# Kernel optimization log

Measured on AMD Instinct MI355X. Metric: run time of the kernel, lower is better.

Reference implementation:

```python
import jax, jax.numpy as jnp
import jax.scipy as jsp
import numpy as np

NUM_EMBEDDINGS = 256
EMBEDDING_DIM = 64
SPARSITY_LEVEL = 4
N_BINS = 16
COEF_MAX = 3.0
COEF_MU = 50.0
COMMITMENT_COST = 0.25
EPSILON = 1e-10


def _normalize_dict(dictionary):
    # F.normalize(dict, p=2, dim=0, eps): x / max(||x||_2, eps) per column
    nrm = jnp.linalg.norm(dictionary, axis=0, keepdims=True)
    return dictionary / jnp.maximum(nrm, EPSILON)


def _quantize_coeff_mu_law(coeff):
    inv_log1p_mu = 1.0 / np.log1p(COEF_MU)  # scalar constant
    c = jnp.clip(coeff, -COEF_MAX, COEF_MAX) / COEF_MAX
    encoded = jnp.sign(c) * jnp.log1p(jnp.abs(c) * COEF_MU) * inv_log1p_mu
    scaled = (encoded + 1.0) * ((N_BINS - 1) / 2.0)
    bin_idx = jnp.clip(jnp.round(scaled).astype(jnp.int32), 0, N_BINS - 1)
    # dequantize
    z = bin_idx.astype(coeff.dtype) * (2.0 / (N_BINS - 1)) - 1.0
    decoded = jnp.sign(z) * (jnp.expm1(jnp.abs(z) / inv_log1p_mu) / COEF_MU) * COEF_MAX
    return bin_idx, decoded


def batch_omp_with_support(X, Dn, K):
    # X: [M, Bs] signals, Dn: [M, N] normalized dictionary
    G = Dn.T @ Dn                       # [N, N] Gram
    h_bar = (Dn.T @ X).T                # [Bs, N] correlations
    Bs, N = h_bar.shape
    dt = h_bar.dtype
    h = h_bar
    mask = jnp.zeros((Bs, N), dtype=bool)
    L = jnp.ones((Bs, 1, 1), dtype=dt)  # incremental Cholesky of G[I, I]
    I = jnp.zeros((Bs, 0), dtype=jnp.int32)
    x_sel = jnp.zeros((Bs, 0), dtype=dt)
    rows = jnp.arange(Bs)
    for k in range(1, K + 1):  # K is small & static -> unrolled
        idx = jnp.argmax(jnp.abs(h) * (~mask), axis=1).astype(jnp.int32)
        mask = mask.at[rows, idx].set(True)
        if k > 1:
            G_stack = G[I, idx[:, None]]                     # [Bs, k-1]
            w = jsp.linalg.solve_triangular(L, G_stack[..., None], lower=True)  # [Bs,k-1,1]
            wT = jnp.swapaxes(w, 1, 2)                       # [Bs,1,k-1]
            w_corner = jnp.sqrt(jnp.clip(1.0 - jnp.sum(wT * wT, axis=2, keepdims=True), 1e-12))
            top = jnp.concatenate([L, jnp.zeros((Bs, k - 1, 1), dt)], axis=2)
            bot = jnp.concatenate([wT, w_corner], axis=2)
            L = jnp.concatenate([top, bot], axis=1)          # [Bs,k,k]
        I = jnp.concatenate([I, idx[:, None]], axis=1)       # [Bs,k]
        h_stack = jnp.take_along_axis(h_bar, I, axis=1)[..., None]  # [Bs,k,1]
        # cholesky_solve: L L^T x = h
        y = jsp.linalg.solve_triangular(L, h_stack, lower=True)
        xs = jsp.linalg.solve_triangular(jnp.swapaxes(L, 1, 2), y, lower=False)
        x_sel = xs[..., 0]                                   # [Bs,k] coeffs aligned w/ support
        beta = jnp.einsum('bk,bkn->bn', x_sel, G[I])         # [Bs,N]
        h = h_bar - beta
    return I, x_sel


def setup_inputs() -> dict:
    key = jax.random.key(0)
    k1, k2 = jax.random.split(key)
    z_e = jax.random.normal(k1, (32, EMBEDDING_DIM, 64, 64), dtype=jnp.float32)
    dictionary = jax.random.normal(k2, (EMBEDDING_DIM, NUM_EMBEDDINGS), dtype=jnp.float32) * 0.02
    return {"z_e": z_e, "dictionary": dictionary}


def reference(z_e, dictionary):
    B, C, H, W = z_e.shape
    Dn = _normalize_dict(dictionary)
    signals = jnp.transpose(z_e, (0, 2, 3, 1)).reshape(-1, C).T  # [C, B*H*W]
    # OMP runs with no grad (torch.no_grad in original)
    support, coeffs = jax.lax.stop_gradient(
        batch_omp_with_support(jax.lax.stop_gradient(signals), jax.lax.stop_gradient(Dn), SPARSITY_LEVEL)
    )
    # mu-law quantize coefficients (constants w.r.t. grads)
    bin_idx, coeffs_q = _quantize_coeff_mu_law(coeffs)
    # reconstruct with quantized coeffs; dictionary path is differentiable
    atoms = Dn.T[support]                                    # [Bs, K, C]
    recon_flat = jnp.einsum('bkc,bk->bc', atoms, coeffs_q)
    recon = jnp.transpose(recon_flat.reshape(B, H, W, C), (0, 3, 1, 2))
    # VQ-VAE style losses + STE
    e_latent_loss = jnp.mean((jax.lax.stop_gradient(recon) - z_e) ** 2)
    q_latent_loss = jnp.mean((recon - jax.lax.stop_gradient(z_e)) ** 2)
    loss = q_latent_loss + COMMITMENT_COST * e_latent_loss
    z_q = z_e + jax.lax.stop_gradient(recon - z_e)
    return z_q, loss


if __name__ == '__main__':
    out = reference(**setup_inputs())
    print(out[0].shape, out[1])
```

## Files before the change

kernel.cpp:

```cpp
#include <hip/hip_runtime.h>
#include <math.h>

#define NEMB 256
#define DIM 64
#define SIGS 128
#define THREADS 512
#define NSIG 131072
#define GRID (NSIG / SIGS)

#define LOG1P50 3.9318256327243257
#define INV_MU_F ((float)(1.0 / LOG1P50))
#define TWO15_F ((float)(2.0 / 15.0))

#define LB_SIG   0
#define LB_XS    32768
#define LB_QI    34816
#define LB_RED   36864
#define LDS_BYTES 36928

__global__ void k_normalize(const float* __restrict__ D, float* __restrict__ Dn)
{
#pragma clang fp contract(off)
    int n = threadIdx.x;
    float ss = 0.0f;
    for (int c = 0; c < DIM; c++) {
        float v = D[c * NEMB + n];
        float sq = v * v;
        ss = ss + sq;
    }
    float nrm = fmaxf(sqrtf(ss), 1e-10f);
    for (int c = 0; c < DIM; c++)
        Dn[c * NEMB + n] = D[c * NEMB + n] / nrm;
}

__global__ void k_gram(const float* __restrict__ Dn, float* __restrict__ G)
{
    __shared__ float coli[DIM];
    int i = blockIdx.x, j = threadIdx.x;
    if (j < DIM) coli[j] = Dn[j * NEMB + i];
    __syncthreads();
    float s = 0.0f;
#pragma unroll
    for (int c = 0; c < DIM; c++) s = fmaf(coli[c], Dn[c * NEMB + j], s);
    G[i * NEMB + j] = s;
}

__device__ __forceinline__ float quant_decode(float coeff)
{
#pragma clang fp contract(off)
    float c = fminf(fmaxf(coeff, -3.0f), 3.0f) / 3.0f;
    float ac = fabsf(c);
    float sgn = (c > 0.0f) ? 1.0f : ((c < 0.0f) ? -1.0f : 0.0f);
    float l = log1pf(ac * 50.0f);
    float enc = (sgn * l) * INV_MU_F;
    float scaled = (enc + 1.0f) * 7.5f;
    int bin = (int)rintf(scaled);
    bin = bin < 0 ? 0 : (bin > 15 ? 15 : bin);
    float t = (float)bin * TWO15_F;
    float zv = t - 1.0f;
    float az = fabsf(zv);
    float sz = (zv > 0.0f) ? 1.0f : ((zv < 0.0f) ? -1.0f : 0.0f);
    float e = expm1f(az / INV_MU_F);
    return (sz * (e / 50.0f)) * 3.0f;
}

__device__ __forceinline__ void omp_signal(const float* hb4, int lane,
                                           const float* __restrict__ G,
                                           float* __restrict__ xsv,
                                           int* __restrict__ qi, int s)
{
#pragma clang fp contract(off)
    float hbsi[4] = {hb4[0], hb4[1], hb4[2], hb4[3]};
    float h[4] = {hbsi[0], hbsi[1], hbsi[2], hbsi[3]};
    float Lm[4][4];
    float Gr[3][4];
    int Iv[4];
    float hsel[4];
    float xs[4];
    float y[4];
    int m4 = 0;
#pragma unroll
    for (int kk = 0; kk < 4; kk++) {
        float bv = -1.0f;
        int bj = 0;
#pragma unroll
        for (int j = 0; j < 4; j++) {
            float v = (m4 & (1 << j)) ? 0.0f : fabsf(h[j]);
            if (v > bv) { bv = v; bj = j; }
        }
        float vmax = bv;
#pragma unroll
        for (int off = 1; off < 64; off <<= 1)
            vmax = fmaxf(vmax, __shfl_xor(vmax, off));
        unsigned long long mball = __ballot(bv == vmax);
        int owner = __ffsll(mball) - 1;
        int idx = __shfl(4 * lane + bj, owner);
        idx = __builtin_amdgcn_readfirstlane(idx);
        if (lane == owner) m4 |= (1 << bj);
        if (kk < 3) {
            const float4 gt = *(const float4*)(G + (size_t)idx * NEMB + 4 * lane);
            Gr[kk][0] = gt.x; Gr[kk][1] = gt.y; Gr[kk][2] = gt.z; Gr[kk][3] = gt.w;
        }
        if (kk > 0) {
            float Gs[3], w[3];
#pragma unroll
            for (int j = 0; j < 3; j++)
                if (j < kk) Gs[j] = G[(size_t)Iv[j] * NEMB + idx];
#pragma unroll
            for (int r = 0; r < 3; r++) {
                if (r < kk) {
                    float acc = 0.0f;
#pragma unroll
                    for (int cc = 0; cc < 3; cc++)
                        if (cc < r) { float p = Lm[r][cc] * w[cc]; acc = acc + p; }
                    float t2 = Gs[r] - acc;
                    w[r] = t2 / Lm[r][r];
                }
            }
            float ssum = 0.0f;
#pragma unroll
            for (int j = 0; j < 3; j++)
                if (j < kk) { float p = w[j] * w[j]; ssum = ssum + p; }
            float om = 1.0f - ssum;
            float wc = sqrtf(fmaxf(om, 1e-12f));
#pragma unroll
            for (int cc = 0; cc < 3; cc++)
                if (cc < kk) Lm[kk][cc] = w[cc];
            Lm[kk][kk] = wc;
        } else {
            Lm[0][0] = 1.0f;
        }
        Iv[kk] = idx;
        {
            float tv = (bj == 0) ? hbsi[0] : ((bj == 1) ? hbsi[1] : ((bj == 2) ? hbsi[2] : hbsi[3]));
            hsel[kk] = __shfl(tv, owner);
        }
        {
            float acc = 0.0f;
#pragma unroll
            for (int cc = 0; cc < 3; cc++)
                if (cc < kk) { float p = Lm[kk][cc] * y[cc]; acc = acc + p; }
            float t2 = hsel[kk] - acc;
            y[kk] = t2 / Lm[kk][kk];
        }
#pragma unroll
        for (int r = 3; r >= 0; r--) {
            if (r <= kk) {
                float acc = 0.0f;
#pragma unroll
                for (int cc = 0; cc < 4; cc++)
                    if (cc > r && cc <= kk) { float p = Lm[cc][r] * xs[cc]; acc = acc + p; }
                float t2 = y[r] - acc;
                xs[r] = t2 / Lm[r][r];
            }
        }
        if (kk < 3) {
#pragma unroll
            for (int j = 0; j < 4; j++) {
                float bsum = 0.0f;
#pragma unroll
                for (int jj = 0; jj < 3; jj++)
                    if (jj <= kk) { float p = xs[jj] * Gr[jj][j]; bsum = bsum + p; }
                h[j] = hbsi[j] - bsum;
            }
        }
    }
    if (lane == 0) {
#pragma unroll
        for (int j = 0; j < 4; j++) {
            xsv[j * SIGS + s] = xs[j];
            qi[j * SIGS + s] = Iv[j];
        }
    }
}

__launch_bounds__(THREADS, 6)
__global__ void k_omp(const float* __restrict__ z,
                      const float* __restrict__ Dn_g,
                      const float* __restrict__ G,
                      double* __restrict__ loss_acc,
                      float* __restrict__ zq)
{
    extern __shared__ char smem[];
    float* sig = (float*)(smem + LB_SIG);
    float* xsv = (float*)(smem + LB_XS);
    int* qi = (int*)(smem + LB_QI);
    double* red = (double*)(smem + LB_RED);

    int tid = threadIdx.x;
    int lane = tid & 63;
    int wid = tid >> 6;

    long sbase = (long)blockIdx.x * SIGS;
    int b = (int)(sbase >> 12);
    int pl0 = (int)(sbase & 4095);
    const float* zb = z + ((size_t)b << 18) + pl0;
    {
        int w = tid & (SIGS - 1);
        int g = tid >> 7;
#pragma unroll
        for (int i = 0; i < 16; i++) {
            int c = g * 16 + i;
            sig[c * SIGS + w] = zb[(size_t)c * 4096 + w];
        }
    }
    __syncthreads();

    for (int g2 = 0; g2 < 2; g2++) {
        int s0 = wid * 16 + g2 * 8;
        float hb[8][4];
#pragma unroll
        for (int a = 0; a < 8; a++)
#pragma unroll
            for (int t = 0; t < 4; t++) hb[a][t] = 0.0f;
#pragma unroll 8
        for (int c = 0; c < DIM; c++) {
            float4 sva = *(const float4*)(sig + c * SIGS + s0);
            float4 svb = *(const float4*)(sig + c * SIGS + s0 + 4);
            float s8[8] = {sva.x, sva.y, sva.z, sva.w, svb.x, svb.y, svb.z, svb.w};
            float4 dv = *(const float4*)(Dn_g + c * NEMB + 4 * lane);
            float d4[4] = {dv.x, dv.y, dv.z, dv.w};
#pragma unroll
            for (int a = 0; a < 8; a++) {
                hb[a][0] = fmaf(s8[a], d4[0], hb[a][0]);
                hb[a][1] = fmaf(s8[a], d4[1], hb[a][1]);
                hb[a][2] = fmaf(s8[a], d4[2], hb[a][2]);
                hb[a][3] = fmaf(s8[a], d4[3], hb[a][3]);
            }
        }
#pragma unroll
        for (int a = 0; a < 8; a++)
            omp_signal(hb[a], lane, G, xsv, qi, s0 + a);
    }
    __syncthreads();

    {
        int jq = tid >> 7;
        int wq = tid & (SIGS - 1);
        xsv[jq * SIGS + wq] = quant_decode(xsv[jq * SIGS + wq]);
    }
    __syncthreads();

    double lsum = 0.0;
    float* zqb = zq + ((size_t)b << 18) + pl0;
    {
#pragma clang fp contract(off)
        int w = tid & (SIGS - 1);
        int g = tid >> 7;
        float q0 = xsv[0 * SIGS + w], q1 = xsv[1 * SIGS + w];
        float q2 = xsv[2 * SIGS + w], q3 = xsv[3 * SIGS + w];
        int i0 = qi[0 * SIGS + w], i1 = qi[1 * SIGS + w];
        int i2 = qi[2 * SIGS + w], i3 = qi[3 * SIGS + w];
#pragma unroll
        for (int ci = 0; ci < 16; ci++) {
            int c = g * 16 + ci;
            const float* dr = Dn_g + c * NEMB;
            float p0 = q0 * dr[i0];
            float p1 = q1 * dr[i1];
            float p2 = q2 * dr[i2];
            float p3 = q3 * dr[i3];
            float r = p0 + p1;
            r = r + p2;
            r = r + p3;
            float zev = sig[c * SIGS + w];
            float d = r - zev;
            float zqv = zev + d;
            lsum += (double)d * (double)d;
            zqb[(size_t)c * 4096 + w] = zqv;
        }
    }
#pragma unroll
    for (int off = 32; off > 0; off >>= 1) lsum += __shfl_xor(lsum, off);
    if (lane == 0) red[wid] = lsum;
    __syncthreads();
    if (tid == 0) {
        double t = 0.0;
#pragma unroll
        for (int i = 0; i < 8; i++) t += red[i];
        atomicAdd(loss_acc, t);
    }
}

__global__ void k_final(const double* __restrict__ loss_acc, float* __restrict__ out)
{
    double m = loss_acc[0] / 8388608.0;
    out[0] = (float)(m + 0.25 * m);
}

extern "C" void kernel_launch(void* const* d_in, const int* in_sizes, int n_in,
                              void* d_out, int out_size, void* d_ws, size_t ws_size,
                              hipStream_t stream)
{
    const float* z = (const float*)d_in[0];
    const float* D = (const float*)d_in[1];
    float* out = (float*)d_out;
    char* ws = (char*)d_ws;
    double* loss_acc = (double*)ws;
    float* Dn = (float*)(ws + 256);
    float* G = (float*)(ws + 256 + 65536);

    hipMemsetAsync(loss_acc, 0, sizeof(double), stream);
    k_normalize<<<1, NEMB, 0, stream>>>(D, Dn);
    k_gram<<<NEMB, NEMB, 0, stream>>>(Dn, G);
    hipFuncSetAttribute(reinterpret_cast<const void*>(k_omp),
                        hipFuncAttributeMaxDynamicSharedMemorySize, LDS_BYTES);
    k_omp<<<GRID, THREADS, LDS_BYTES, stream>>>(z, Dn, G, loss_acc, out);
    k_final<<<1, 1, 0, stream>>>(loss_acc, out + 8388608);
    (void)in_sizes; (void)n_in; (void)out_size; (void)ws_size;
}
```

Measured before the change: 302.6 us.

## Interleave two OMP signals per wave with DPP reductions and packed FMA

Result: faster. 292.3 us (-3.4%).

```diff
diff --git a/kernel.cpp b/kernel.cpp
--- a/kernel.cpp
+++ b/kernel.cpp
@@ -18,10 +18,37 @@
 #define LB_RED   36864
 #define LDS_BYTES 36928
 
-__global__ void k_normalize(const float* __restrict__ D, float* __restrict__ Dn)
+typedef float f2 __attribute__((ext_vector_type(2)));
+
+__device__ __forceinline__ float rdlane_f(float v, int lane)
+{
+    return __builtin_bit_cast(float, __builtin_amdgcn_readlane(__builtin_bit_cast(int, v), lane));
+}
+
+template<int CTRL>
+__device__ __forceinline__ float dpp_fmax(float m)
+{
+    int sh = __builtin_amdgcn_update_dpp(0, __builtin_bit_cast(int, m), CTRL, 0xf, 0xf, true);
+    return fmaxf(m, __builtin_bit_cast(float, sh));
+}
+
+__device__ __forceinline__ float wave_max_nn(float v)
+{
+    v = dpp_fmax<0x111>(v);
+    v = dpp_fmax<0x112>(v);
+    v = dpp_fmax<0x114>(v);
+    v = dpp_fmax<0x118>(v);
+    v = dpp_fmax<0x142>(v);
+    v = dpp_fmax<0x143>(v);
+    return v;
+}
+
+__global__ void k_normalize(const float* __restrict__ D, float* __restrict__ Dn,
+                            double* __restrict__ loss_acc, unsigned int* __restrict__ ctr)
 {
 #pragma clang fp contract(off)
     int n = threadIdx.x;
+    if (n == 0) { loss_acc[0] = 0.0; ctr[0] = 0u; }
     float ss = 0.0f;
     for (int c = 0; c < DIM; c++) {
         float v = D[c * NEMB + n];
@@ -64,48 +91,84 @@
     return (sz * (e / 50.0f)) * 3.0f;
 }
 
-__device__ __forceinline__ void omp_signal(const float* hb4, int lane,
-                                           const float* __restrict__ G,
-                                           float* __restrict__ xsv,
-                                           int* __restrict__ qi, int s)
+__device__ __forceinline__ void omp_pair(const f2* hbA_in, const f2* hbB_in,
+                                         int lane, int hi,
+                                         const float* __restrict__ G,
+                                         float* __restrict__ xsv,
+                                         int* __restrict__ qi, int sA)
 {
 #pragma clang fp contract(off)
-    float hbsi[4] = {hb4[0], hb4[1], hb4[2], hb4[3]};
-    float h[4] = {hbsi[0], hbsi[1], hbsi[2], hbsi[3]};
+    f2 hbsiA[2] = {hbA_in[0], hbA_in[1]};
+    f2 hbsiB[2] = {hbB_in[0], hbB_in[1]};
+    f2 hA[2] = {hbsiA[0], hbsiA[1]};
+    f2 hB[2] = {hbsiB[0], hbsiB[1]};
+    f2 GrA[3][2], GrB[3][2];
     float Lm[4][4];
-    float Gr[3][4];
-    int Iv[4];
-    float hsel[4];
-    float xs[4];
-    float y[4];
-    int m4 = 0;
+    int IvA[4], IvB[4];
+    float y[4], xs[4];
+    int m4A = 0, m4B = 0;
 #pragma unroll
     for (int kk = 0; kk < 4; kk++) {
-        float bv = -1.0f;
-        int bj = 0;
+        float bvA = -1.0f, bvB = -1.0f;
+        int bjA = 0, bjB = 0;
 #pragma unroll
         for (int j = 0; j < 4; j++) {
-            float v = (m4 & (1 << j)) ? 0.0f : fabsf(h[j]);
-            if (v > bv) { bv = v; bj = j; }
-        }
-        float vmax = bv;
-#pragma unroll
-        for (int off = 1; off < 64; off <<= 1)
-            vmax = fmaxf(vmax, __shfl_xor(vmax, off));
-        unsigned long long mball = __ballot(bv == vmax);
-        int owner = __ffsll(mball) - 1;
-        int idx = __shfl(4 * lane + bj, owner);
-        idx = __builtin_amdgcn_readfirstlane(idx);
-        if (lane == owner) m4 |= (1 << bj);
+            float vA_ = (m4A & (1 << j)) ? 0.0f : fabsf(hA[j >> 1][j & 1]);
+            if (vA_ > bvA) { bvA = vA_; bjA = j; }
+            float vB_ = (m4B & (1 << j)) ? 0.0f : fabsf(hB[j >> 1][j & 1]);
+            if (vB_ > bvB) { bvB = vB_; bjB = j; }
+        }
+        float mA = wave_max_nn(bvA);
+        float mB = wave_max_nn(bvB);
+        float vmaxA = rdlane_f(mA, 63);
+        float vmaxB = rdlane_f(mB, 63);
+        unsigned long long ballA = __ballot(bvA == vmaxA);
+        unsigned long long ballB = __ballot(bvB == vmaxB);
+        int ownerA = __ffsll((long long)ballA) - 1;
+        int ownerB = __ffsll((long long)ballB) - 1;
+        int bjAo = __builtin_amdgcn_readlane(bjA, ownerA);
+        int bjBo = __builtin_amdgcn_readlane(bjB, ownerB);
+        int idxA = 4 * ownerA + bjAo;
+        int idxB = 4 * ownerB + bjBo;
+        m4A |= (lane == ownerA) ? (1 << bjAo) : 0;
+        m4B |= (lane == ownerB) ? (1 << bjBo) : 0;
+        IvA[kk] = idxA; IvB[kk] = idxB;
+        float tvA = hbsiA[0][0];
+        tvA = (bjA == 1) ? hbsiA[0][1] : tvA;
+        tvA = (bjA == 2) ? hbsiA[1][0] : tvA;
+        tvA = (bjA == 3) ? hbsiA[1][1] : tvA;
+        float tvB = hbsiB[0][0];
+        tvB = (bjB == 1) ? hbsiB[0][1] : tvB;
+        tvB = (bjB == 2) ? hbsiB[1][0] : tvB;
+        tvB = (bjB == 3) ? hbsiB[1][1] : tvB;
+        float hselA = rdlane_f(tvA, ownerA);
+        float hselB = rdlane_f(tvB, ownerB);
+        float hsel = hi ? hselB : hselA;
         if (kk < 3) {
-            const float4 gt = *(const float4*)(G + (size_t)idx * NEMB + 4 * lane);
-            Gr[kk][0] = gt.x; Gr[kk][1] = gt.y; Gr[kk][2] = gt.z; Gr[kk][3] = gt.w;
+            const float4 ga = *(const float4*)(G + ((size_t)idxA << 8) + 4 * lane);
+            const float4 gb = *(const float4*)(G + ((size_t)idxB << 8) + 4 * lane);
+            GrA[kk][0].x = ga.x; GrA[kk][0].y = ga.y;
+            GrA[kk][1].x = ga.z; GrA[kk][1].y = ga.w;
+            GrB[kk][0].x = gb.x; GrB[kk][0].y = gb.y;
+            GrB[kk][1].x = gb.z; GrB[kk][1].y = gb.w;
         }
         if (kk > 0) {
             float Gs[3], w[3];
 #pragma unroll
             for (int j = 0; j < 3; j++)
-                if (j < kk) Gs[j] = G[(size_t)Iv[j] * NEMB + idx];
+                if (j < kk) {
+                    float eA = GrA[j][0][0];
+                    eA = (bjAo == 1) ? GrA[j][0][1] : eA;
+                    eA = (bjAo == 2) ? GrA[j][1][0] : eA;
+                    eA = (bjAo == 3) ? GrA[j][1][1] : eA;
+                    float eB = GrB[j][0][0];
+                    eB = (bjBo == 1) ? GrB[j][0][1] : eB;
+                    eB = (bjBo == 2) ? GrB[j][1][0] : eB;
+                    eB = (bjBo == 3) ? GrB[j][1][1] : eB;
+                    float gA = rdlane_f(eA, ownerA);
+                    float gB = rdlane_f(eB, ownerB);
+                    Gs[j] = hi ? gB : gA;
+                }
 #pragma unroll
             for (int r = 0; r < 3; r++) {
                 if (r < kk) {
@@ -114,7 +177,7 @@
                     for (int cc = 0; cc < 3; cc++)
                         if (cc < r) { float p = Lm[r][cc] * w[cc]; acc = acc + p; }
                     float t2 = Gs[r] - acc;
-                    w[r] = t2 / Lm[r][r];
+                    w[r] = (r == 0) ? t2 : t2 / Lm[r][r];
                 }
             }
             float ssum = 0.0f;
@@ -130,18 +193,13 @@
         } else {
             Lm[0][0] = 1.0f;
         }
-        Iv[kk] = idx;
-        {
-            float tv = (bj == 0) ? hbsi[0] : ((bj == 1) ? hbsi[1] : ((bj == 2) ? hbsi[2] : hbsi[3]));
-            hsel[kk] = __shfl(tv, owner);
-        }
         {
             float acc = 0.0f;
 #pragma unroll
             for (int cc = 0; cc < 3; cc++)
                 if (cc < kk) { float p = Lm[kk][cc] * y[cc]; acc = acc + p; }
-            float t2 = hsel[kk] - acc;
-            y[kk] = t2 / Lm[kk][kk];
+            float t2 = hsel - acc;
+            y[kk] = (kk == 0) ? t2 : t2 / Lm[kk][kk];
         }
 #pragma unroll
         for (int r = 3; r >= 0; r--) {
@@ -151,35 +209,54 @@
                 for (int cc = 0; cc < 4; cc++)
                     if (cc > r && cc <= kk) { float p = Lm[cc][r] * xs[cc]; acc = acc + p; }
                 float t2 = y[r] - acc;
-                xs[r] = t2 / Lm[r][r];
+                xs[r] = (r == 0) ? t2 : t2 / Lm[r][r];
             }
         }
         if (kk < 3) {
-#pragma unroll
-            for (int j = 0; j < 4; j++) {
-                float bsum = 0.0f;
+            float xsA[4], xsB[4];
+#pragma unroll
+            for (int j = 0; j < 4; j++)
+                if (j <= kk) {
+                    xsA[j] = rdlane_f(xs[j], 0);
+                    xsB[j] = rdlane_f(xs[j], 32);
+                }
+#pragma unroll
+            for (int jp = 0; jp < 2; jp++) {
+                f2 bsA = {0.0f, 0.0f};
+                f2 bsB = {0.0f, 0.0f};
 #pragma unroll
                 for (int jj = 0; jj < 3; jj++)
-                    if (jj <= kk) { float p = xs[jj] * Gr[jj][j]; bsum = bsum + p; }
-                h[j] = hbsi[j] - bsum;
+                    if (jj <= kk) {
+                        f2 xa = {xsA[jj], xsA[jj]};
+                        f2 xb = {xsB[jj], xsB[jj]};
+                        f2 pA = xa * GrA[jj][jp];
+                        bsA = bsA + pA;
+                        f2 pB = xb * GrB[jj][jp];
+                        bsB = bsB + pB;
+                    }
+                hA[jp] = hbsiA[jp] - bsA;
+                hB[jp] = hbsiB[jp] - bsB;
             }
         }
     }
-    if (lane == 0) {
+    if ((lane & 31) == 0) {
+        int s = sA + hi;
 #pragma unroll
         for (int j = 0; j < 4; j++) {
             xsv[j * SIGS + s] = xs[j];
-            qi[j * SIGS + s] = Iv[j];
-        }
-    }
-}
-
-__launch_bounds__(THREADS, 6)
+            qi[j * SIGS + s] = hi ? IvB[j] : IvA[j];
+        }
+    }
+}
+
+__launch_bounds__(THREADS, 4)
 __global__ void k_omp(const float* __restrict__ z,
                       const float* __restrict__ Dn_g,
                       const float* __restrict__ G,
                       double* __restrict__ loss_acc,
-                      float* __restrict__ zq)
+                      unsigned int* __restrict__ ctr,
+                      float* __restrict__ zq,
+                      float* __restrict__ loss_out)
 {
     extern __shared__ char smem[];
     float* sig = (float*)(smem + LB_SIG);
@@ -189,6 +266,7 @@
 
     int tid = threadIdx.x;
     int lane = tid & 63;
+    int hi = lane >> 5;
     int wid = tid >> 6;
 
     long sbase = (long)blockIdx.x * SIGS;
@@ -208,29 +286,30 @@
 
     for (int g2 = 0; g2 < 2; g2++) {
         int s0 = wid * 16 + g2 * 8;
-        float hb[8][4];
-#pragma unroll
-        for (int a = 0; a < 8; a++)
-#pragma unroll
-            for (int t = 0; t < 4; t++) hb[a][t] = 0.0f;
+        f2 hb[8][2];
+#pragma unroll
+        for (int a = 0; a < 8; a++) {
+            hb[a][0] = (f2){0.0f, 0.0f};
+            hb[a][1] = (f2){0.0f, 0.0f};
+        }
 #pragma unroll 8
         for (int c = 0; c < DIM; c++) {
             float4 sva = *(const float4*)(sig + c * SIGS + s0);
             float4 svb = *(const float4*)(sig + c * SIGS + s0 + 4);
             float s8[8] = {sva.x, sva.y, sva.z, sva.w, svb.x, svb.y, svb.z, svb.w};
             float4 dv = *(const float4*)(Dn_g + c * NEMB + 4 * lane);
-            float d4[4] = {dv.x, dv.y, dv.z, dv.w};
+            f2 d0; d0.x = dv.x; d0.y = dv.y;
+            f2 d1; d1.x = dv.z; d1.y = dv.w;
 #pragma unroll
             for (int a = 0; a < 8; a++) {
-                hb[a][0] = fmaf(s8[a], d4[0], hb[a][0]);
-                hb[a][1] = fmaf(s8[a], d4[1], hb[a][1]);
-                hb[a][2] = fmaf(s8[a], d4[2], hb[a][2]);
-                hb[a][3] = fmaf(s8[a], d4[3], hb[a][3]);
+                f2 sa = {s8[a], s8[a]};
+                hb[a][0] = __builtin_elementwise_fma(sa, d0, hb[a][0]);
+                hb[a][1] = __builtin_elementwise_fma(sa, d1, hb[a][1]);
             }
         }
 #pragma unroll
-        for (int a = 0; a < 8; a++)
-            omp_signal(hb[a], lane, G, xsv, qi, s0 + a);
+        for (int p = 0; p < 4; p++)
+            omp_pair(hb[2 * p], hb[2 * p + 1], lane, hi, G, xsv, qi, s0 + 2 * p);
     }
     __syncthreads();
 
@@ -278,13 +357,13 @@
 #pragma unroll
         for (int i = 0; i < 8; i++) t += red[i];
         atomicAdd(loss_acc, t);
-    }
-}
-
-__global__ void k_final(const double* __restrict__ loss_acc, float* __restrict__ out)
-{
-    double m = loss_acc[0] / 8388608.0;
-    out[0] = (float)(m + 0.25 * m);
+        __threadfence();
+        unsigned int done = atomicAdd(ctr, 1u);
+        if (done == GRID - 1) {
+            double m = atomicAdd(loss_acc, 0.0) / 8388608.0;
+            loss_out[0] = (float)(m + 0.25 * m);
+        }
+    }
 }
 
 extern "C" void kernel_launch(void* const* d_in, const int* in_sizes, int n_in,
@@ -296,15 +375,14 @@
     float* out = (float*)d_out;
     char* ws = (char*)d_ws;
     double* loss_acc = (double*)ws;
+    unsigned int* ctr = (unsigned int*)(ws + 8);
     float* Dn = (float*)(ws + 256);
     float* G = (float*)(ws + 256 + 65536);
 
-    hipMemsetAsync(loss_acc, 0, sizeof(double), stream);
-    k_normalize<<<1, NEMB, 0, stream>>>(D, Dn);
+    k_normalize<<<1, NEMB, 0, stream>>>(D, Dn, loss_acc, ctr);
     k_gram<<<NEMB, NEMB, 0, stream>>>(Dn, G);
     hipFuncSetAttribute(reinterpret_cast<const void*>(k_omp),
                         hipFuncAttributeMaxDynamicSharedMemorySize, LDS_BYTES);
-    k_omp<<<GRID, THREADS, LDS_BYTES, stream>>>(z, Dn, G, loss_acc, out);
-    k_final<<<1, 1, 0, stream>>>(loss_acc, out + 8388608);
+    k_omp<<<GRID, THREADS, LDS_BYTES, stream>>>(z, Dn, G, loss_acc, ctr, out, out + 8388608);
     (void)in_sizes; (void)n_in; (void)out_size; (void)ws_size;
 }
```

## Process four signals per wavefront with 16-lane groups and DPP argmax reductions

Applied to the files above, without the earlier changes.

After: 644.6 us. +113.0%, slower.

```diff
diff --git a/kernel.cpp b/kernel.cpp
--- a/kernel.cpp
+++ b/kernel.cpp
@@ -18,10 +18,38 @@
 #define LB_RED   36864
 #define LDS_BYTES 36928
 
-__global__ void k_normalize(const float* __restrict__ D, float* __restrict__ Dn)
+typedef float f2 __attribute__((ext_vector_type(2)));
+
+template<int CTRL>
+__device__ __forceinline__ void red_step(float& bv, float& bh, int& gi)
+{
+    float bv2 = __builtin_bit_cast(float,
+        __builtin_amdgcn_update_dpp(0, __builtin_bit_cast(int, bv), CTRL, 0xf, 0xf, true));
+    float bh2 = __builtin_bit_cast(float,
+        __builtin_amdgcn_update_dpp(0, __builtin_bit_cast(int, bh), CTRL, 0xf, 0xf, true));
+    int gi2 = __builtin_amdgcn_update_dpp(0, gi, CTRL, 0xf, 0xf, true);
+    bool take = (bv2 > bv) || ((bv2 == bv) && (gi2 < gi));
+    bv = take ? bv2 : bv;
+    bh = take ? bh2 : bh;
+    gi = take ? gi2 : gi;
+}
+
+__device__ __forceinline__ float swz16_f(float v)
+{
+    return __builtin_bit_cast(float,
+        __builtin_amdgcn_ds_swizzle(__builtin_bit_cast(int, v), 0x01F0));
+}
+__device__ __forceinline__ int swz16_i(int v)
+{
+    return __builtin_amdgcn_ds_swizzle(v, 0x01F0);
+}
+
+__global__ void k_normalize(const float* __restrict__ D, float* __restrict__ Dn,
+                            double* __restrict__ loss_acc, unsigned int* __restrict__ ctr)
 {
 #pragma clang fp contract(off)
     int n = threadIdx.x;
+    if (n == 0) { loss_acc[0] = 0.0; ctr[0] = 0u; }
     float ss = 0.0f;
     for (int c = 0; c < DIM; c++) {
         float v = D[c * NEMB + n];
@@ -64,123 +92,16 @@
     return (sz * (e / 50.0f)) * 3.0f;
 }
 
-__device__ __forceinline__ void omp_signal(const float* hb4, int lane,
-                                           const float* __restrict__ G,
-                                           float* __restrict__ xsv,
-                                           int* __restrict__ qi, int s)
-{
-#pragma clang fp contract(off)
-    float hbsi[4] = {hb4[0], hb4[1], hb4[2], hb4[3]};
-    float h[4] = {hbsi[0], hbsi[1], hbsi[2], hbsi[3]};
-    float Lm[4][4];
-    float Gr[3][4];
-    int Iv[4];
-    float hsel[4];
-    float xs[4];
-    float y[4];
-    int m4 = 0;
-#pragma unroll
-    for (int kk = 0; kk < 4; kk++) {
-        float bv = -1.0f;
-        int bj = 0;
-#pragma unroll
-        for (int j = 0; j < 4; j++) {
-            float v = (m4 & (1 << j)) ? 0.0f : fabsf(h[j]);
-            if (v > bv) { bv = v; bj = j; }
-        }
-        float vmax = bv;
-#pragma unroll
-        for (int off = 1; off < 64; off <<= 1)
-            vmax = fmaxf(vmax, __shfl_xor(vmax, off));
-        unsigned long long mball = __ballot(bv == vmax);
-        int owner = __ffsll(mball) - 1;
-        int idx = __shfl(4 * lane + bj, owner);
-        idx = __builtin_amdgcn_readfirstlane(idx);
-        if (lane == owner) m4 |= (1 << bj);
-        if (kk < 3) {
-            const float4 gt = *(const float4*)(G + (size_t)idx * NEMB + 4 * lane);
-            Gr[kk][0] = gt.x; Gr[kk][1] = gt.y; Gr[kk][2] = gt.z; Gr[kk][3] = gt.w;
-        }
-        if (kk > 0) {
-            float Gs[3], w[3];
-#pragma unroll
-            for (int j = 0; j < 3; j++)
-                if (j < kk) Gs[j] = G[(size_t)Iv[j] * NEMB + idx];
-#pragma unroll
-            for (int r = 0; r < 3; r++) {
-                if (r < kk) {
-                    float acc = 0.0f;
-#pragma unroll
-                    for (int cc = 0; cc < 3; cc++)
-                        if (cc < r) { float p = Lm[r][cc] * w[cc]; acc = acc + p; }
-                    float t2 = Gs[r] - acc;
-                    w[r] = t2 / Lm[r][r];
-                }
-            }
-            float ssum = 0.0f;
-#pragma unroll
-            for (int j = 0; j < 3; j++)
-                if (j < kk) { float p = w[j] * w[j]; ssum = ssum + p; }
-            float om = 1.0f - ssum;
-            float wc = sqrtf(fmaxf(om, 1e-12f));
-#pragma unroll
-            for (int cc = 0; cc < 3; cc++)
-                if (cc < kk) Lm[kk][cc] = w[cc];
-            Lm[kk][kk] = wc;
-        } else {
-            Lm[0][0] = 1.0f;
-        }
-        Iv[kk] = idx;
-        {
-            float tv = (bj == 0) ? hbsi[0] : ((bj == 1) ? hbsi[1] : ((bj == 2) ? hbsi[2] : hbsi[3]));
-            hsel[kk] = __shfl(tv, owner);
-        }
-        {
-            float acc = 0.0f;
-#pragma unroll
-            for (int cc = 0; cc < 3; cc++)
-                if (cc < kk) { float p = Lm[kk][cc] * y[cc]; acc = acc + p; }
-            float t2 = hsel[kk] - acc;
-            y[kk] = t2 / Lm[kk][kk];
-        }
-#pragma unroll
-        for (int r = 3; r >= 0; r--) {
-            if (r <= kk) {
-                float acc = 0.0f;
-#pragma unroll
-                for (int cc = 0; cc < 4; cc++)
-                    if (cc > r && cc <= kk) { float p = Lm[cc][r] * xs[cc]; acc = acc + p; }
-                float t2 = y[r] - acc;
-                xs[r] = t2 / Lm[r][r];
-            }
-        }
-        if (kk < 3) {
-#pragma unroll
-            for (int j = 0; j < 4; j++) {
-                float bsum = 0.0f;
-#pragma unroll
-                for (int jj = 0; jj < 3; jj++)
-                    if (jj <= kk) { float p = xs[jj] * Gr[jj][j]; bsum = bsum + p; }
-                h[j] = hbsi[j] - bsum;
-            }
-        }
-    }
-    if (lane == 0) {
-#pragma unroll
-        for (int j = 0; j < 4; j++) {
-            xsv[j * SIGS + s] = xs[j];
-            qi[j * SIGS + s] = Iv[j];
-        }
-    }
-}
-
-__launch_bounds__(THREADS, 6)
+__launch_bounds__(THREADS, 4)
 __global__ void k_omp(const float* __restrict__ z,
                       const float* __restrict__ Dn_g,
                       const float* __restrict__ G,
                       double* __restrict__ loss_acc,
-                      float* __restrict__ zq)
-{
+                      unsigned int* __restrict__ ctr,
+                      float* __restrict__ zq,
+                      float* __restrict__ loss_out)
+{
+#pragma clang fp contract(off)
     extern __shared__ char smem[];
     float* sig = (float*)(smem + LB_SIG);
     float* xsv = (float*)(smem + LB_XS);
@@ -190,6 +111,9 @@
     int tid = threadIdx.x;
     int lane = tid & 63;
     int wid = tid >> 6;
+    int q = lane & 15;
+    int g = lane >> 4;
+    int q16 = q << 4;
 
     long sbase = (long)blockIdx.x * SIGS;
     int b = (int)(sbase >> 12);
@@ -197,40 +121,176 @@
     const float* zb = z + ((size_t)b << 18) + pl0;
     {
         int w = tid & (SIGS - 1);
-        int g = tid >> 7;
+        int gg = tid >> 7;
 #pragma unroll
         for (int i = 0; i < 16; i++) {
-            int c = g * 16 + i;
+            int c = gg * 16 + i;
             sig[c * SIGS + w] = zb[(size_t)c * 4096 + w];
         }
     }
     __syncthreads();
 
-    for (int g2 = 0; g2 < 2; g2++) {
-        int s0 = wid * 16 + g2 * 8;
-        float hb[8][4];
-#pragma unroll
-        for (int a = 0; a < 8; a++)
-#pragma unroll
-            for (int t = 0; t < 4; t++) hb[a][t] = 0.0f;
-#pragma unroll 8
+    for (int quad = 0; quad < 4; quad++) {
+        int s = wid * 16 + quad * 4 + g;
+        f2 hb[8];
+#pragma unroll
+        for (int i = 0; i < 8; i++) hb[i] = (f2){0.0f, 0.0f};
+#pragma unroll 4
         for (int c = 0; c < DIM; c++) {
-            float4 sva = *(const float4*)(sig + c * SIGS + s0);
-            float4 svb = *(const float4*)(sig + c * SIGS + s0 + 4);
-            float s8[8] = {sva.x, sva.y, sva.z, sva.w, svb.x, svb.y, svb.z, svb.w};
-            float4 dv = *(const float4*)(Dn_g + c * NEMB + 4 * lane);
-            float d4[4] = {dv.x, dv.y, dv.z, dv.w};
-#pragma unroll
-            for (int a = 0; a < 8; a++) {
-                hb[a][0] = fmaf(s8[a], d4[0], hb[a][0]);
-                hb[a][1] = fmaf(s8[a], d4[1], hb[a][1]);
-                hb[a][2] = fmaf(s8[a], d4[2], hb[a][2]);
-                hb[a][3] = fmaf(s8[a], d4[3], hb[a][3]);
-            }
-        }
-#pragma unroll
-        for (int a = 0; a < 8; a++)
-            omp_signal(hb[a], lane, G, xsv, qi, s0 + a);
+            float xc = sig[c * SIGS + s];
+            const float4* dp = (const float4*)(Dn_g + c * NEMB + q16);
+            float4 d0 = dp[0], d1 = dp[1], d2 = dp[2], d3 = dp[3];
+            f2 sv = {xc, xc};
+            hb[0] = __builtin_elementwise_fma(sv, (f2){d0.x, d0.y}, hb[0]);
+            hb[1] = __builtin_elementwise_fma(sv, (f2){d0.z, d0.w}, hb[1]);
+            hb[2] = __builtin_elementwise_fma(sv, (f2){d1.x, d1.y}, hb[2]);
+            hb[3] = __builtin_elementwise_fma(sv, (f2){d1.z, d1.w}, hb[3]);
+            hb[4] = __builtin_elementwise_fma(sv, (f2){d2.x, d2.y}, hb[4]);
+            hb[5] = __builtin_elementwise_fma(sv, (f2){d2.z, d2.w}, hb[5]);
+            hb[6] = __builtin_elementwise_fma(sv, (f2){d3.x, d3.y}, hb[6]);
+            hb[7] = __builtin_elementwise_fma(sv, (f2){d3.z, d3.w}, hb[7]);
+        }
+
+        float scanv[16];
+#pragma unroll
+        for (int j = 0; j < 16; j++) scanv[j] = fabsf(hb[j >> 1][j & 1]);
+
+        int msel = 0;
+        float L10, L11, L20, L21, L22, L30, L31, L32, L33;
+        float y0, y1, y2, y3;
+        float x0 = 0.f, x1 = 0.f, x2 = 0.f, x3 = 0.f;
+        int Iv0 = 0, Iv1 = 0, Iv2 = 0, Iv3 = 0;
+        f2 gr[3][8];
+
+#pragma unroll
+        for (int kk = 0; kk < 4; kk++) {
+            float bv = -1.0f, bh = 0.0f;
+            int gi = 0;
+#pragma unroll
+            for (int j = 0; j < 16; j++) {
+                float av = scanv[j];
+                bool t = av > bv;
+                bv = t ? av : bv;
+                bh = t ? hb[j >> 1][j & 1] : bh;
+                gi = t ? (q16 + j) : gi;
+            }
+            red_step<0xB1>(bv, bh, gi);
+            red_step<0x4E>(bv, bh, gi);
+            red_step<0x114>(bv, bh, gi);
+            red_step<0x118>(bv, bh, gi);
+            bh = swz16_f(bh);
+            gi = swz16_i(gi);
+            float hsel = bh;
+
+            float Gs0 = 0.f, Gs1 = 0.f, Gs2 = 0.f;
+            if (kk > 0) Gs0 = G[(Iv0 << 8) + gi];
+            if (kk > 1) Gs1 = G[(Iv1 << 8) + gi];
+            if (kk > 2) Gs2 = G[(Iv2 << 8) + gi];
+            if (kk < 3) {
+                const float4* grp = (const float4*)(G + ((size_t)gi << 8) + q16);
+                float4 ra = grp[0], rb = grp[1], rc = grp[2], rd = grp[3];
+                gr[kk][0] = (f2){ra.x, ra.y};  gr[kk][1] = (f2){ra.z, ra.w};
+                gr[kk][2] = (f2){rb.x, rb.y};  gr[kk][3] = (f2){rb.z, rb.w};
+                gr[kk][4] = (f2){rc.x, rc.y};  gr[kk][5] = (f2){rc.z, rc.w};
+                gr[kk][6] = (f2){rd.x, rd.y};  gr[kk][7] = (f2){rd.z, rd.w};
+            }
+            {
+                int bit = 1 << (gi & 15);
+                msel |= ((gi >> 4) == q) ? bit : 0;
+            }
+            if (kk == 0) Iv0 = gi;
+            if (kk == 1) Iv1 = gi;
+            if (kk == 2) Iv2 = gi;
+            if (kk == 3) Iv3 = gi;
+
+            if (kk == 1) {
+                float w0 = Gs0;
+                float ss = w0 * w0;
+                float om = 1.0f - ss;
+                L10 = w0;
+                L11 = sqrtf(fmaxf(om, 1e-12f));
+            }
+            if (kk == 2) {
+                float w0 = Gs0;
+                float t2 = Gs1 - L10 * w0;
+                float w1 = t2 / L11;
+                float ss = w0 * w0;
+                float p = w1 * w1; ss = ss + p;
+                float om = 1.0f - ss;
+                L20 = w0; L21 = w1;
+                L22 = sqrtf(fmaxf(om, 1e-12f));
+            }
+            if (kk == 3) {
+                float w0 = Gs0;
+                float t2 = Gs1 - L10 * w0;
+                float w1 = t2 / L11;
+                float acc = L20 * w0;
+                float p = L21 * w1; acc = acc + p;
+                float t3 = Gs2 - acc;
+                float w2 = t3 / L22;
+                float ss = w0 * w0;
+                p = w1 * w1; ss = ss + p;
+                p = w2 * w2; ss = ss + p;
+                float om = 1.0f - ss;
+                L30 = w0; L31 = w1; L32 = w2;
+                L33 = sqrtf(fmaxf(om, 1e-12f));
+            }
+            if (kk == 0) y0 = hsel;
+            if (kk == 1) { float a = L10 * y0; y1 = (hsel - a) / L11; }
+            if (kk == 2) { float a = L20 * y0; float p = L21 * y1; a = a + p;
+                           y2 = (hsel - a) / L22; }
+            if (kk == 3) { float a = L30 * y0; float p = L31 * y1; a = a + p;
+                           p = L32 * y2; a = a + p;
+                           y3 = (hsel - a) / L33; }
+            if (kk == 0) { x0 = y0; }
+            if (kk == 1) {
+                x1 = y1 / L11;
+                float a = L10 * x1;
+                x0 = y0 - a;
+            }
+            if (kk == 2) {
+                x2 = y2 / L22;
+                float a = L21 * x2;
+                x1 = (y1 - a) / L11;
+                a = L10 * x1;
+                float p = L20 * x2; a = a + p;
+                x0 = y0 - a;
+            }
+            if (kk == 3) {
+                x3 = y3 / L33;
+                float a = L32 * x3;
+                x2 = (y2 - a) / L22;
+                a = L21 * x2;
+                float p = L31 * x3; a = a + p;
+                x1 = (y1 - a) / L11;
+                a = L10 * x1;
+                p = L20 * x2; a = a + p;
+                p = L30 * x3; a = a + p;
+                x0 = y0 - a;
+            }
+            if (kk < 3) {
+                f2 xv0 = {x0, x0};
+                f2 xv1 = {x1, x1};
+                f2 xv2 = {x2, x2};
+#pragma unroll
+                for (int i = 0; i < 8; i++) {
+                    f2 bsum = xv0 * gr[0][i];
+                    if (kk > 0) { f2 pp = xv1 * gr[1][i]; bsum = bsum + pp; }
+                    if (kk > 1) { f2 pp = xv2 * gr[2][i]; bsum = bsum + pp; }
+                    f2 hres = hb[i] - bsum;
+                    float a0 = fabsf(hres[0]);
+                    float a1 = fabsf(hres[1]);
+                    scanv[2 * i]     = (msel & (1 << (2 * i)))     ? 0.0f : a0;
+                    scanv[2 * i + 1] = (msel & (1 << (2 * i + 1))) ? 0.0f : a1;
+                }
+            }
+        }
+        if (q == 0) {
+            xsv[0 * SIGS + s] = x0; xsv[1 * SIGS + s] = x1;
+            xsv[2 * SIGS + s] = x2; xsv[3 * SIGS + s] = x3;
+            qi[0 * SIGS + s] = Iv0; qi[1 * SIGS + s] = Iv1;
+            qi[2 * SIGS + s] = Iv2; qi[3 * SIGS + s] = Iv3;
+        }
     }
     __syncthreads();
 
@@ -244,16 +304,15 @@
     double lsum = 0.0;
     float* zqb = zq + ((size_t)b << 18) + pl0;
     {
-#pragma clang fp contract(off)
         int w = tid & (SIGS - 1);
-        int g = tid >> 7;
+        int gg = tid >> 7;
         float q0 = xsv[0 * SIGS + w], q1 = xsv[1 * SIGS + w];
         float q2 = xsv[2 * SIGS + w], q3 = xsv[3 * SIGS + w];
         int i0 = qi[0 * SIGS + w], i1 = qi[1 * SIGS + w];
         int i2 = qi[2 * SIGS + w], i3 = qi[3 * SIGS + w];
 #pragma unroll
         for (int ci = 0; ci < 16; ci++) {
-            int c = g * 16 + ci;
+            int c = gg * 16 + ci;
             const float* dr = Dn_g + c * NEMB;
             float p0 = q0 * dr[i0];
             float p1 = q1 * dr[i1];
@@ -278,13 +337,13 @@
 #pragma unroll
         for (int i = 0; i < 8; i++) t += red[i];
         atomicAdd(loss_acc, t);
-    }
-}
-
-__global__ void k_final(const double* __restrict__ loss_acc, float* __restrict__ out)
-{
-    double m = loss_acc[0] / 8388608.0;
-    out[0] = (float)(m + 0.25 * m);
+        __threadfence();
+        unsigned int done = atomicAdd(ctr, 1u);
+        if (done == GRID - 1) {
+            double m = atomicAdd(loss_acc, 0.0) / 8388608.0;
+            loss_out[0] = (float)(m + 0.25 * m);
+        }
+    }
 }
 
 extern "C" void kernel_launch(void* const* d_in, const int* in_sizes, int n_in,
@@ -296,15 +355,14 @@
     float* out = (float*)d_out;
     char* ws = (char*)d_ws;
     double* loss_acc = (double*)ws;
+    unsigned int* ctr = (unsigned int*)(ws + 8);
     float* Dn = (float*)(ws + 256);
     float* G = (float*)(ws + 256 + 65536);
 
-    hipMemsetAsync(loss_acc, 0, sizeof(double), stream);
-    k_normalize<<<1, NEMB, 0, stream>>>(D, Dn);
+    k_normalize<<<1, NEMB, 0, stream>>>(D, Dn, loss_acc, ctr);
     k_gram<<<NEMB, NEMB, 0, stream>>>(Dn, G);
     hipFuncSetAttribute(reinterpret_cast<const void*>(k_omp),
                         hipFuncAttributeMaxDynamicSharedMemorySize, LDS_BYTES);
-    k_omp<<<GRID, THREADS, LDS_BYTES, stream>>>(z, Dn, G, loss_acc, out);
-    k_final<<<1, 1, 0, stream>>>(loss_acc, out + 8388608);
+    k_omp<<<GRID, THREADS, LDS_BYTES, stream>>>(z, Dn, G, loss_acc, ctr, out, out + 8388608);
     (void)in_sizes; (void)n_in; (void)out_size; (void)ws_size;
 }
```
